# Kernel optimization log

Measured on AMD Instinct MI355X. Metric: run time of the kernel, lower is better.

Reference implementation:

```python
import jax, jax.numpy as jnp
import numpy as np
import math

HIDDEN = 768
HEADS = 12
HEAD_DIM = HIDDEN // HEADS  # 64
SEQ = 197
K_RANK = min(128, HEAD_DIM)  # 64
BATCH = 64


def setup_inputs() -> dict:
    key = jax.random.key(0)
    ks = jax.random.split(key, 12)
    init = 0.02
    # Linear weights stored [in, out] (equivalent to torch W.T)
    return {
        "hidden_states": jax.random.normal(ks[0], (BATCH, SEQ, HIDDEN), dtype=jnp.float32),
        "Wq": jax.random.normal(ks[1], (HIDDEN, HIDDEN), dtype=jnp.float32) * init,
        "bq": jnp.zeros((HIDDEN,), dtype=jnp.float32),
        "Wk": jax.random.normal(ks[2], (HIDDEN, HIDDEN), dtype=jnp.float32) * init,
        "bk": jnp.zeros((HIDDEN,), dtype=jnp.float32),
        "Wv": jax.random.normal(ks[3], (HIDDEN, HIDDEN), dtype=jnp.float32) * init,
        "bv": jnp.zeros((HIDDEN,), dtype=jnp.float32),
        "Wo": jax.random.normal(ks[4], (HIDDEN, HIDDEN), dtype=jnp.float32) * init,
        "bo": jnp.zeros((HIDDEN,), dtype=jnp.float32),
        "E_k": jax.random.normal(ks[5], (SEQ, K_RANK), dtype=jnp.float32) * init,
        "E_v": jax.random.normal(ks[6], (SEQ, K_RANK), dtype=jnp.float32) * init,
    }


def reference(hidden_states, Wq, bq, Wk, bk, Wv, bv, Wo, bo, E_k, E_v):
    B, S, D = hidden_states.shape
    H, d = HEADS, HEAD_DIM
    scale = 1.0 / math.sqrt(d)

    def split_heads(x):  # [B,S,D] -> [B,H,S,d]
        return x.reshape(B, S, H, d).transpose(0, 2, 1, 3)

    q = split_heads(hidden_states @ Wq + bq)
    k = split_heads(hidden_states @ Wk + bk)
    v = split_heads(hidden_states @ Wv + bv)

    # low-rank projection of K/V along the sequence axis: [B,H,k,d]
    pk = jnp.einsum('sk,bhsd->bhkd', E_k, k)
    pv = jnp.einsum('sk,bhsd->bhkd', E_v, v)

    # scores over reduced axis: [B,H,S,k]
    scores = jnp.einsum('bhsd,bhkd->bhsk', q, pk) * scale
    probs = jax.nn.softmax(scores, axis=-1)

    ctx = jnp.einsum('bhsk,bhkd->bhsd', probs, pv)
    ctx = ctx.transpose(0, 2, 1, 3).reshape(B, S, D)
    out = ctx @ Wo + bo  # dropout rate 0.0 -> identity
    return out
```

## Files before the change

kernel.cpp:

```cpp
#include <hip/hip_runtime.h>
#include <math.h>

#define B_   64
#define S_   197
#define D_   768
#define H_   12
#define HD_  64
#define M_   (B_ * S_)
#define MPAD 12672
#define KE   224
#define BH_  (B_ * H_)
#define WSZ  ((size_t)D_ * D_)

typedef _Float16 half8_t __attribute__((ext_vector_type(8)));
typedef _Float16 half4_t __attribute__((ext_vector_type(4)));
typedef _Float16 half2_t __attribute__((ext_vector_type(2)));
typedef float floatx4 __attribute__((ext_vector_type(4)));

#define LDS_DMA16(gptr, lptr) \
  __builtin_amdgcn_global_load_lds((const __attribute__((address_space(1))) void*)(gptr), \
                                   (__attribute__((address_space(3))) void*)(lptr), 16, 0, 0)

__global__ __launch_bounds__(256) void prep_y_kernel(
    const float* __restrict__ X,
    const float* __restrict__ Wq, const float* __restrict__ Wk,
    const float* __restrict__ Wv, const float* __restrict__ Wo,
    const float* __restrict__ Ek, const float* __restrict__ Ev,
    _Float16* __restrict__ Xh,
    _Float16* __restrict__ Tcat, _Float16* __restrict__ To,
    float* __restrict__ esumK, float* __restrict__ esumV,
    _Float16* __restrict__ Ybuf)
{
    __shared__ _Float16 smem[KE * 66];
    const int bid = blockIdx.x, tid = threadIdx.x;

    if (bid >= 768 && bid < 3072) {
        const int idx = bid - 768;
        float (*tile)[33] = (float (*)[33])smem;
        const int z = idx / 576, rem = idx % 576;
        const int bx = rem % 24, by = rem / 24;
        const float* W = (z == 0) ? Wk : (z == 1) ? Wv : (z == 2) ? Wq : Wo;
        _Float16* T = (z < 3) ? (Tcat + (size_t)z * WSZ) : To;
        const int n0 = bx * 32, k0 = by * 32;
        const int r = tid >> 3, c4 = (tid & 7) * 4;
        *(float4*)&tile[r][c4] = *(const float4*)&W[(size_t)(k0 + r) * D_ + n0 + c4];
        __syncthreads();
        half4_t o = { (_Float16)tile[c4 + 0][r], (_Float16)tile[c4 + 1][r],
                      (_Float16)tile[c4 + 2][r], (_Float16)tile[c4 + 3][r] };
        *(half4_t*)&T[(size_t)(n0 + r) * D_ + k0 + c4] = o;
        return;
    }

    if (bid >= 3096) {
        const int idx = bid - 3096;
        const float* E = idx ? Ev : Ek;
        float* es = idx ? esumV : esumK;
        if (tid < 64) {
            float acc = 0.f;
            for (int s = 0; s < S_; ++s) acc += E[s * 64 + tid];
            es[tid] = acc;
        }
        return;
    }

    if (bid >= 3072) {
        const int idx = bid - 3072;
        const half8_t z8 = {};
        *(half8_t*)&Xh[(size_t)M_ * D_ + (size_t)(idx * 256 + tid) * 8] = z8;
        return;
    }

    _Float16* Xs = smem;
    const int idx = bid;
    const int b = idx / 12, n0 = (idx % 12) * 64;
    const int w = tid >> 6, lane = tid & 63;
    const int l15 = lane & 15, quad = lane >> 4;

    #pragma unroll
    for (int i = 0; i < 7; ++i) {
        const int s = i * 32 + (tid >> 3);
        const int d0 = (tid & 7) * 8;
        float4 v0 = make_float4(0.f, 0.f, 0.f, 0.f), v1 = v0;
        if (s < S_) {
            const float* src = &X[(size_t)(b * S_ + s) * D_ + n0 + d0];
            v0 = *(const float4*)src;
            v1 = *(const float4*)(src + 4);
        }
        const half8_t h8 = { (_Float16)v0.x, (_Float16)v0.y, (_Float16)v0.z,
                             (_Float16)v0.w, (_Float16)v1.x, (_Float16)v1.y,
                             (_Float16)v1.z, (_Float16)v1.w };
        if (s < S_)
            *(half8_t*)&Xh[(size_t)(b * S_ + s) * D_ + n0 + d0] = h8;
        #pragma unroll
        for (int jj = 0; jj < 4; ++jj) {
            half2_t t2 = { h8[2 * jj], h8[2 * jj + 1] };
            *(half2_t*)&Xs[s * 66 + d0 + 2 * jj] = t2;
        }
    }
    __syncthreads();

    floatx4 acc[2][4] = {};
    #pragma unroll
    for (int k7 = 0; k7 < 7; ++k7) {
        half8_t af[2];
        #pragma unroll
        for (int mi = 0; mi < 2; ++mi) {
            const int row = w * 32 + mi * 16 + l15;
            const float* Esrc = (row < 64) ? Ek : Ev;
            const int er = row & 63;
            #pragma unroll
            for (int jj = 0; jj < 8; ++jj) {
                const int s = k7 * 32 + quad * 8 + jj;
                af[mi][jj] = (_Float16)((s < S_) ? Esrc[s * 64 + er] : 0.f);
            }
        }
        #pragma unroll
        for (int ni = 0; ni < 4; ++ni) {
            const int sb = k7 * 32 + quad * 8;
            half8_t bf;
            #pragma unroll
            for (int jj = 0; jj < 8; ++jj) bf[jj] = Xs[(sb + jj) * 66 + ni * 16 + l15];
            #pragma unroll
            for (int mi = 0; mi < 2; ++mi)
                acc[mi][ni] = __builtin_amdgcn_mfma_f32_16x16x32_f16(
                    af[mi], bf, acc[mi][ni], 0, 0, 0);
        }
    }

    #pragma unroll
    for (int mi = 0; mi < 2; ++mi)
        #pragma unroll
        for (int ni = 0; ni < 4; ++ni)
            #pragma unroll
            for (int i = 0; i < 4; ++i) {
                const int m_local = w * 32 + mi * 16 + quad * 4 + i;
                const int row = (m_local >> 6) * 4096 + b * 64 + (m_local & 63);
                Ybuf[(size_t)row * D_ + n0 + ni * 16 + l15] = (_Float16)acc[mi][ni][i];
            }
}

__global__ __launch_bounds__(256) void gemm_qpkv(
    const _Float16* __restrict__ Xh, const _Float16* __restrict__ Ybuf,
    const _Float16* __restrict__ Tcat,
    const float* __restrict__ bq, const float* __restrict__ bk,
    const float* __restrict__ bv,
    const float* __restrict__ esumK, const float* __restrict__ esumV,
    _Float16* __restrict__ Qh, _Float16* __restrict__ pk16,
    _Float16* __restrict__ pvT)
{
    __shared__ _Float16 sm[32768];
    const int bid = blockIdx.x;
    const _Float16 *A, *W;
    const float *bias, *esum;
    _Float16* O16;
    int m0, n0, rowb;
    bool pvt = false;
    if (bid < 624) {
        const int xcd = bid & 7, t = bid >> 3;
        const int slot = t / 6, j = t - slot * 6;
        const int m_blk = slot * 8 + xcd;
        if (m_blk >= MPAD / 128) return;
        m0 = m_blk * 128; n0 = j * 128; rowb = m0;
        A = Xh; W = Tcat + 2 * WSZ + (size_t)n0 * D_;
        bias = bq; esum = nullptr; O16 = Qh;
    } else {
        const int b2 = bid - 624;
        const int xcd = b2 & 7, t = b2 >> 3;
        const int slot = t / 6, j = t - slot * 6;
        const int m_blk = slot * 8 + xcd;
        m0 = m_blk * 128; n0 = j * 128;
        const bool pv = (m_blk >= 32);
        pvt = pv;
        rowb = pv ? m0 - 4096 : m0;
        A = Ybuf; W = Tcat + (pv ? WSZ : 0) + (size_t)n0 * D_;
        bias = pv ? bv : bk; esum = pv ? esumV : esumK;
        O16 = pk16;
    }

    const int tid = threadIdx.x;
    const int w = tid >> 6, lane = tid & 63;
    const int fr = lane & 15, quad = lane >> 4, f7 = lane & 7;
    const int l3 = lane >> 3;
    const int csrc = ((lane & 7) ^ l3) * 8;
    const int wm = (w >> 1) * 64, wn = (w & 1) * 64;

    const _Float16* Abase = A + (size_t)(m0 + w * 32 + l3) * D_ + csrc;
    const _Float16* Wbase = W + (size_t)(w * 32 + l3) * D_ + csrc;

    floatx4 acc[4][4] = {};

#define QPKV_STAGE(BUF, K0) \
    { _Pragma("unroll") \
      for (int j = 0; j < 4; ++j) { \
          LDS_DMA16(Abase + (size_t)(j * 8) * D_ + (K0), &sm[(BUF) * 16384 + w * 2048 + j * 512]); \
          LDS_DMA16(Wbase + (size_t)(j * 8) * D_ + (K0), &sm[(BUF) * 16384 + 8192 + w * 2048 + j * 512]); \
      } }

#define QPKV_COMPUTE(BUF) \
    { _Pragma("unroll") \
      for (int ksub = 0; ksub < 2; ++ksub) { \
          const int sa = ((ksub * 4 + quad) ^ f7) * 8; \
          half8_t af[4], bf[4]; \
          _Pragma("unroll") \
          for (int i = 0; i < 4; ++i) { \
              af[i] = *(const half8_t*)&sm[(BUF) * 16384 + (wm + i * 16 + fr) * 64 + sa]; \
              bf[i] = *(const half8_t*)&sm[(BUF) * 16384 + 8192 + (wn + i * 16 + fr) * 64 + sa]; \
          } \
          _Pragma("unroll") \
          for (int mi = 0; mi < 4; ++mi) \
              _Pragma("unroll") \
              for (int ni = 0; ni < 4; ++ni) \
                  acc[mi][ni] = __builtin_amdgcn_mfma_f32_16x16x32_f16( \
                      af[mi], bf[ni], acc[mi][ni], 0, 0, 0); \
      } }

    QPKV_STAGE(0, 0);
    __syncthreads();
    #pragma unroll
    for (int t = 0; t < 10; t += 2) {
        QPKV_STAGE(1, (t + 1) * 64);
        QPKV_COMPUTE(0);
        __syncthreads();
        QPKV_STAGE(0, (t + 2) * 64);
        QPKV_COMPUTE(1);
        __syncthreads();
    }
    QPKV_STAGE(1, 11 * 64);
    QPKV_COMPUTE(0);
    __syncthreads();
    QPKV_COMPUTE(1);

    float bval[4];
    #pragma unroll
    for (int ni = 0; ni < 4; ++ni)
        bval[ni] = bias[n0 + wn + ni * 16 + fr];

    _Float16* ct = &sm[w * 2176];

    if (pvt) {
        #pragma unroll
        for (int half = 0; half < 2; ++half) {
            #pragma unroll
            for (int ni2 = 0; ni2 < 2; ++ni2) {
                const int ni = half * 2 + ni2;
                #pragma unroll
                for (int mi = 0; mi < 4; ++mi) {
                    const float4 es4 = *(const float4*)&esum[mi * 16 + quad * 4];
                    const float esv[4] = { es4.x, es4.y, es4.z, es4.w };
                    #pragma unroll
                    for (int i = 0; i < 4; ++i)
                        ct[(ni2 * 16 + fr) * 68 + mi * 16 + quad * 4 + i] =
                            (_Float16)(acc[mi][ni][i] + esv[i] * bval[ni]);
                }
            }
            #pragma unroll
            for (int pass = 0; pass < 4; ++pass) {
                const int rr = pass * 8 + (lane >> 3);
                const int cc = (lane & 7) * 8;
                const half8_t v = *(const half8_t*)&ct[rr * 68 + cc];
                *(half8_t*)&pvT[(size_t)(n0 + wn + half * 32 + rr) * 4096
                                + rowb + wm + cc] = v;
            }
        }
        return;
    }

    #pragma unroll
    for (int half = 0; half < 2; ++half) {
        #pragma unroll
        for (int mi2 = 0; mi2 < 2; ++mi2) {
            const int mi = half * 2 + mi2;
            float esv[4] = {1.f, 1.f, 1.f, 1.f};
            if (esum) {
                const float4 es4 = *(const float4*)&esum[mi * 16 + quad * 4];
                esv[0] = es4.x; esv[1] = es4.y; esv[2] = es4.z; esv[3] = es4.w;
            }
            #pragma unroll
            for (int ni = 0; ni < 4; ++ni)
                #pragma unroll
                for (int i = 0; i < 4; ++i)
                    ct[(mi2 * 16 + quad * 4 + i) * 68 + ni * 16 + fr] =
                        (_Float16)(acc[mi][ni][i] + esv[i] * bval[ni]);
        }
        #pragma unroll
        for (int pass = 0; pass < 4; ++pass) {
            const int rr = pass * 8 + (lane >> 3);
            const int cc = (lane & 7) * 8;
            const half8_t v = *(const half8_t*)&ct[rr * 68 + cc];
            *(half8_t*)&O16[(size_t)(rowb + wm + half * 32 + rr) * D_ + n0 + wn + cc] = v;
        }
    }
}

__global__ __launch_bounds__(256) void gemm_o(
    const _Float16* __restrict__ CTX, const _Float16* __restrict__ To,
    const float* __restrict__ bo, float* __restrict__ O32)
{
    __shared__ _Float16 sm[32768];
    const int xcd = blockIdx.x & 7, t = blockIdx.x >> 3;
    const int slot = t / 6, j = t - slot * 6;
    const int m_blk = slot * 8 + xcd;
    if (m_blk >= MPAD / 128) return;
    const int m0 = m_blk * 128, n0 = j * 128;

    const int tid = threadIdx.x;
    const int w = tid >> 6, lane = tid & 63;
    const int fr = lane & 15, quad = lane >> 4, f7 = lane & 7;
    const int l3 = lane >> 3;
    const int csrc = ((lane & 7) ^ l3) * 8;
    const int wm = (w >> 1) * 64, wn = (w & 1) * 64;

    const _Float16* Abase = CTX + (size_t)(m0 + w * 32 + l3) * D_ + csrc;
    const _Float16* Wbase = To + (size_t)(n0 + w * 32 + l3) * D_ + csrc;

    floatx4 acc[4][4] = {};

    QPKV_STAGE(0, 0);
    __syncthreads();
    #pragma unroll
    for (int t2 = 0; t2 < 10; t2 += 2) {
        QPKV_STAGE(1, (t2 + 1) * 64);
        QPKV_COMPUTE(0);
        __syncthreads();
        QPKV_STAGE(0, (t2 + 2) * 64);
        QPKV_COMPUTE(1);
        __syncthreads();
    }
    QPKV_STAGE(1, 11 * 64);
    QPKV_COMPUTE(0);
    __syncthreads();
    QPKV_COMPUTE(1);

    float bval[4];
    #pragma unroll
    for (int ni = 0; ni < 4; ++ni)
        bval[ni] = bo[n0 + wn + ni * 16 + fr];

    const bool full = (m0 + 128 <= M_);
    #pragma unroll
    for (int ni = 0; ni < 4; ++ni) {
        const int n = n0 + wn + ni * 16 + fr;
        #pragma unroll
        for (int mi = 0; mi < 4; ++mi)
            #pragma unroll
            for (int i = 0; i < 4; ++i) {
                const int m = m0 + wm + mi * 16 + quad * 4 + i;
                if (full || m < M_)
                    O32[(size_t)m * D_ + n] = acc[mi][ni][i] + bval[ni];
            }
    }
}

__global__ __launch_bounds__(256) void attn_kernel(
    const _Float16* __restrict__ Qh, const _Float16* __restrict__ pk16,
    const _Float16* __restrict__ pvT, _Float16* __restrict__ CTXh)
{
    __shared__ _Float16 P[64 * 80];
    const int bh = blockIdx.x, b = bh / H_, h = bh % H_;
    const int tid = threadIdx.x, w = tid >> 6, lane = tid & 63;
    const int l15 = lane & 15, quad = lane >> 4;
    const _Float16* pkB = pk16 + (size_t)(b * 64) * D_ + h * 64;
    const _Float16* pvB = pvT + (size_t)(h * 64) * 4096 + b * 64;
    const size_t qbase = (size_t)(b * S_) * D_ + h * HD_;

    half8_t bkf[4][2], bvf[4][2];
    #pragma unroll
    for (int ni = 0; ni < 4; ++ni)
        #pragma unroll
        for (int kk = 0; kk < 2; ++kk) {
            bkf[ni][kk] = *(const half8_t*)&pkB[(size_t)(ni * 16 + l15) * D_ + kk * 32 + quad * 8];
            bvf[ni][kk] = *(const half8_t*)&pvB[(size_t)(ni * 16 + l15) * 4096 + kk * 32 + quad * 8];
        }

    for (int t = w; t < 13; t += 4) {
        const int srow = t * 16;
        floatx4 acc[4] = {};
        #pragma unroll
        for (int kk = 0; kk < 2; ++kk) {
            const half8_t aq = *(const half8_t*)
                &Qh[qbase + (size_t)(srow + l15) * D_ + kk * 32 + quad * 8];
            #pragma unroll
            for (int ni = 0; ni < 4; ++ni)
                acc[ni] = __builtin_amdgcn_mfma_f32_16x16x32_f16(
                    aq, bkf[ni][kk], acc[ni], 0, 0, 0);
        }
        float p[4][4];
        #pragma unroll
        for (int i = 0; i < 4; ++i) {
            const float s0 = acc[0][i] * 0.125f, s1 = acc[1][i] * 0.125f;
            const float s2 = acc[2][i] * 0.125f, s3 = acc[3][i] * 0.125f;
            float mx = fmaxf(fmaxf(s0, s1), fmaxf(s2, s3));
            #pragma unroll
            for (int off = 1; off < 16; off <<= 1)
                mx = fmaxf(mx, __shfl_xor(mx, off, 64));
            const float e0 = __expf(s0 - mx), e1 = __expf(s1 - mx);
            const float e2 = __expf(s2 - mx), e3 = __expf(s3 - mx);
            float sme = e0 + e1 + e2 + e3;
            #pragma unroll
            for (int off = 1; off < 16; off <<= 1)
                sme += __shfl_xor(sme, off, 64);
            const float inv = 1.f / sme;
            p[0][i] = e0 * inv; p[1][i] = e1 * inv;
            p[2][i] = e2 * inv; p[3][i] = e3 * inv;
        }
        #pragma unroll
        for (int ni = 0; ni < 4; ++ni)
            #pragma unroll
            for (int i = 0; i < 4; ++i)
                P[(w * 16 + quad * 4 + i) * 80 + ni * 16 + l15] = (_Float16)p[ni][i];

        floatx4 accv[4] = {};
        #pragma unroll
        for (int kk = 0; kk < 2; ++kk) {
            const half8_t ap = *(const half8_t*)&P[(w * 16 + l15) * 80 + kk * 32 + quad * 8];
            #pragma unroll
            for (int ni = 0; ni < 4; ++ni)
                accv[ni] = __builtin_amdgcn_mfma_f32_16x16x32_f16(
                    ap, bvf[ni][kk], accv[ni], 0, 0, 0);
        }
        #pragma unroll
        for (int ni = 0; ni < 4; ++ni)
            #pragma unroll
            for (int i = 0; i < 4; ++i) {
                const int s = srow + quad * 4 + i;
                if (s < S_)
                    CTXh[qbase + (size_t)s * D_ + ni * 16 + l15] = (_Float16)accv[ni][i];
            }
    }
}

extern "C" void kernel_launch(void* const* d_in, const int* in_sizes, int n_in,
                              void* d_out, int out_size, void* d_ws, size_t ws_size,
                              hipStream_t stream) {
    const float* X   = (const float*)d_in[0];
    const float* Wq  = (const float*)d_in[1];
    const float* bq  = (const float*)d_in[2];
    const float* Wk  = (const float*)d_in[3];
    const float* bk  = (const float*)d_in[4];
    const float* Wv  = (const float*)d_in[5];
    const float* bv  = (const float*)d_in[6];
    const float* Wo  = (const float*)d_in[7];
    const float* bo  = (const float*)d_in[8];
    const float* E_k = (const float*)d_in[9];
    const float* E_v = (const float*)d_in[10];
    float* out = (float*)d_out;

    char* p = (char*)d_ws;
    _Float16* Xh   = (_Float16*)p; p += (size_t)MPAD * D_ * 2;
    _Float16* Tcat = (_Float16*)p; p += (size_t)3 * WSZ * 2;
    _Float16* To   = (_Float16*)p; p += (size_t)WSZ * 2;
    _Float16* Qh   = (_Float16*)p; p += (size_t)MPAD * D_ * 2;
    float* esumK   = (float*)p;    p += 64 * sizeof(float);
    float* esumV   = (float*)p;    p += 64 * sizeof(float);
    _Float16* Ybuf = (_Float16*)p; p += (size_t)8192 * D_ * 2;
    _Float16* pk16 = (_Float16*)p; p += (size_t)4096 * D_ * 2;
    _Float16* pvT  = (_Float16*)p;

    prep_y_kernel<<<3098, 256, 0, stream>>>(X, Wq, Wk, Wv, Wo, E_k, E_v,
                                            Xh, Tcat, To, esumK, esumV, Ybuf);
    gemm_qpkv<<<1008, 256, 0, stream>>>(Xh, Ybuf, Tcat,
                                        bq, bk, bv, esumK, esumV,
                                        Qh, pk16, pvT);
    attn_kernel<<<BH_, 256, 0, stream>>>(Qh, pk16, pvT, Xh);
    gemm_o<<<624, 256, 0, stream>>>(Xh, To, bo, out);
}
```

Before: 196.5 us.

## Use triple-buffered K=32 LDS pipeline with explicit vmcnt waits in GEMMs

```diff
diff --git a/kernel.cpp b/kernel.cpp
--- a/kernel.cpp
+++ b/kernel.cpp
@@ -20,6 +20,12 @@
 #define LDS_DMA16(gptr, lptr) \
   __builtin_amdgcn_global_load_lds((const __attribute__((address_space(1))) void*)(gptr), \
                                    (__attribute__((address_space(3))) void*)(lptr), 16, 0, 0)
+
+#define VMCNT(n) do { asm volatile("s_waitcnt vmcnt(" n ")" ::: "memory"); \
+                      __builtin_amdgcn_sched_barrier(0); } while (0)
+#define BARRIER() do { __builtin_amdgcn_sched_barrier(0); \
+                       __builtin_amdgcn_s_barrier(); \
+                       __builtin_amdgcn_sched_barrier(0); } while (0)
 
 __global__ __launch_bounds__(256) void prep_y_kernel(
     const float* __restrict__ X,
@@ -139,6 +145,43 @@
             }
 }
 
+#define STG32(BUF, T) \
+    { _Pragma("unroll") \
+      for (int j = 0; j < 2; ++j) { \
+          LDS_DMA16(Abase + (size_t)(j * 16) * D_ + (T) * 32, \
+                    &sm[(BUF) * 8192 + w * 1024 + j * 512]); \
+          LDS_DMA16(Wbase + (size_t)(j * 16) * D_ + (T) * 32, \
+                    &sm[(BUF) * 8192 + 4096 + w * 1024 + j * 512]); \
+      } }
+
+#define CMP32(BUF) \
+    { const int sa = (quad ^ (fr & 3)) * 8; \
+      half8_t af[4], bf[4]; \
+      _Pragma("unroll") \
+      for (int i = 0; i < 4; ++i) { \
+          af[i] = *(const half8_t*)&sm[(BUF) * 8192 + (wm + i * 16 + fr) * 32 + sa]; \
+          bf[i] = *(const half8_t*)&sm[(BUF) * 8192 + 4096 + (wn + i * 16 + fr) * 32 + sa]; \
+      } \
+      _Pragma("unroll") \
+      for (int mi = 0; mi < 4; ++mi) \
+          _Pragma("unroll") \
+          for (int ni = 0; ni < 4; ++ni) \
+              acc[mi][ni] = __builtin_amdgcn_mfma_f32_16x16x32_f16( \
+                  af[mi], bf[ni], acc[mi][ni], 0, 0, 0); }
+
+#define PIPE24() \
+    STG32(0, 0); STG32(1, 1); \
+    _Pragma("unroll") \
+    for (int t = 0; t < 22; ++t) { \
+        VMCNT("4"); BARRIER(); \
+        STG32((t + 2) % 3, t + 2); \
+        CMP32(t % 3); \
+    } \
+    VMCNT("4"); BARRIER(); \
+    CMP32(1); \
+    VMCNT("0"); BARRIER(); \
+    CMP32(2);
+
 __global__ __launch_bounds__(256) void gemm_qpkv(
     const _Float16* __restrict__ Xh, const _Float16* __restrict__ Ybuf,
     const _Float16* __restrict__ Tcat,
@@ -148,7 +191,7 @@
     _Float16* __restrict__ Qh, _Float16* __restrict__ pk16,
     _Float16* __restrict__ pvT)
 {
-    __shared__ _Float16 sm[32768];
+    __shared__ _Float16 sm[24576];
     const int bid = blockIdx.x;
     const _Float16 *A, *W;
     const float *bias, *esum;
@@ -179,56 +222,17 @@
 
     const int tid = threadIdx.x;
     const int w = tid >> 6, lane = tid & 63;
-    const int fr = lane & 15, quad = lane >> 4, f7 = lane & 7;
-    const int l3 = lane >> 3;
-    const int csrc = ((lane & 7) ^ l3) * 8;
+    const int fr = lane & 15, quad = lane >> 4;
+    const int l2 = lane >> 2;
+    const int c8 = ((lane & 3) ^ (l2 & 3)) * 8;
     const int wm = (w >> 1) * 64, wn = (w & 1) * 64;
 
-    const _Float16* Abase = A + (size_t)(m0 + w * 32 + l3) * D_ + csrc;
-    const _Float16* Wbase = W + (size_t)(w * 32 + l3) * D_ + csrc;
+    const _Float16* Abase = A + (size_t)(m0 + w * 32 + l2) * D_ + c8;
+    const _Float16* Wbase = W + (size_t)(w * 32 + l2) * D_ + c8;
 
     floatx4 acc[4][4] = {};
 
-#define QPKV_STAGE(BUF, K0) \
-    { _Pragma("unroll") \
-      for (int j = 0; j < 4; ++j) { \
-          LDS_DMA16(Abase + (size_t)(j * 8) * D_ + (K0), &sm[(BUF) * 16384 + w * 2048 + j * 512]); \
-          LDS_DMA16(Wbase + (size_t)(j * 8) * D_ + (K0), &sm[(BUF) * 16384 + 8192 + w * 2048 + j * 512]); \
-      } }
-
-#define QPKV_COMPUTE(BUF) \
-    { _Pragma("unroll") \
-      for (int ksub = 0; ksub < 2; ++ksub) { \
-          const int sa = ((ksub * 4 + quad) ^ f7) * 8; \
-          half8_t af[4], bf[4]; \
-          _Pragma("unroll") \
-          for (int i = 0; i < 4; ++i) { \
-              af[i] = *(const half8_t*)&sm[(BUF) * 16384 + (wm + i * 16 + fr) * 64 + sa]; \
-              bf[i] = *(const half8_t*)&sm[(BUF) * 16384 + 8192 + (wn + i * 16 + fr) * 64 + sa]; \
-          } \
-          _Pragma("unroll") \
-          for (int mi = 0; mi < 4; ++mi) \
-              _Pragma("unroll") \
-              for (int ni = 0; ni < 4; ++ni) \
-                  acc[mi][ni] = __builtin_amdgcn_mfma_f32_16x16x32_f16( \
-                      af[mi], bf[ni], acc[mi][ni], 0, 0, 0); \
-      } }
-
-    QPKV_STAGE(0, 0);
-    __syncthreads();
-    #pragma unroll
-    for (int t = 0; t < 10; t += 2) {
-        QPKV_STAGE(1, (t + 1) * 64);
-        QPKV_COMPUTE(0);
-        __syncthreads();
-        QPKV_STAGE(0, (t + 2) * 64);
-        QPKV_COMPUTE(1);
-        __syncthreads();
-    }
-    QPKV_STAGE(1, 11 * 64);
-    QPKV_COMPUTE(0);
-    __syncthreads();
-    QPKV_COMPUTE(1);
+    PIPE24();
 
     float bval[4];
     #pragma unroll
@@ -296,7 +300,7 @@
     const _Float16* __restrict__ CTX, const _Float16* __restrict__ To,
     const float* __restrict__ bo, float* __restrict__ O32)
 {
-    __shared__ _Float16 sm[32768];
+    __shared__ _Float16 sm[24576];
     const int xcd = blockIdx.x & 7, t = blockIdx.x >> 3;
     const int slot = t / 6, j = t - slot * 6;
     const int m_blk = slot * 8 + xcd;
@@ -305,31 +309,17 @@
 
     const int tid = threadIdx.x;
     const int w = tid >> 6, lane = tid & 63;
-    const int fr = lane & 15, quad = lane >> 4, f7 = lane & 7;
-    const int l3 = lane >> 3;
-    const int csrc = ((lane & 7) ^ l3) * 8;
+    const int fr = lane & 15, quad = lane >> 4;
+    const int l2 = lane >> 2;
+    const int c8 = ((lane & 3) ^ (l2 & 3)) * 8;
     const int wm = (w >> 1) * 64, wn = (w & 1) * 64;
 
-    const _Float16* Abase = CTX + (size_t)(m0 + w * 32 + l3) * D_ + csrc;
-    const _Float16* Wbase = To + (size_t)(n0 + w * 32 + l3) * D_ + csrc;
+    const _Float16* Abase = CTX + (size_t)(m0 + w * 32 + l2) * D_ + c8;
+    const _Float16* Wbase = To + (size_t)(n0 + w * 32 + l2) * D_ + c8;
 
     floatx4 acc[4][4] = {};
 
-    QPKV_STAGE(0, 0);
-    __syncthreads();
-    #pragma unroll
-    for (int t2 = 0; t2 < 10; t2 += 2) {
-        QPKV_STAGE(1, (t2 + 1) * 64);
-        QPKV_COMPUTE(0);
-        __syncthreads();
-        QPKV_STAGE(0, (t2 + 2) * 64);
-        QPKV_COMPUTE(1);
-        __syncthreads();
-    }
-    QPKV_STAGE(1, 11 * 64);
-    QPKV_COMPUTE(0);
-    __syncthreads();
-    QPKV_COMPUTE(1);
+    PIPE24();
 
     float bval[4];
     #pragma unroll
```

New measurement: 201.2 us. 2.4% more time.
